# Kernel tuning notes

Measured on AMD Instinct MI355X. Metric: run time of the kernel, lower is better.

Reference implementation:

```python
import jax, jax.numpy as jnp
import numpy as np

B, K, D_MODEL = 64, 256, 512
D_STATE, D_CONV, EXPAND = 16, 4, 1
D_INNER = EXPAND * D_MODEL
DT_RANK = (D_MODEL + 15) // 16  # 32
EPS = 1e-5


def _layer_norm(x, g, b):
    m = jnp.mean(x, axis=-1, keepdims=True)
    v = jnp.mean(jnp.square(x - m), axis=-1, keepdims=True)
    return (x - m) * jax.lax.rsqrt(v + EPS) * g + b


def _silu(x):
    return x * jax.nn.sigmoid(x)


def _mamba_block(x, in_proj_w, conv_w, conv_b, x_proj_w, dt_proj_w, dt_proj_b, A_log, Dp, out_proj_w):
    # x: (B, K, d_model)
    b, k, _ = x.shape
    d_inner = A_log.shape[0]
    d_state = A_log.shape[1]
    dt_rank = dt_proj_w.shape[1]
    xz = x @ in_proj_w.T                      # (B, K, 2*d_inner)
    xi, z = jnp.split(xz, 2, axis=-1)
    # causal depthwise conv1d, width d_conv
    pad = conv_w.shape[1] - 1
    xp = jnp.pad(xi, ((0, 0), (pad, 0), (0, 0)))
    xc = conv_b + sum(xp[:, w:w + k, :] * conv_w[:, w] for w in range(conv_w.shape[1]))
    xc = _silu(xc)
    proj = xc @ x_proj_w.T                    # (B, K, dt_rank + 2*d_state)
    dtr = proj[..., :dt_rank]
    Bc = proj[..., dt_rank:dt_rank + d_state]  # (B, K, d_state)
    Cc = proj[..., dt_rank + d_state:]         # (B, K, d_state)
    dt = jax.nn.softplus(dtr @ dt_proj_w.T + dt_proj_b)  # (B, K, d_inner)
    A = -jnp.exp(A_log)                       # (d_inner, d_state)

    def step(h, inp):
        dt_t, x_t, B_t, C_t = inp             # (B,d_inner),(B,d_inner),(B,d_state),(B,d_state)
        dA = jnp.exp(dt_t[:, :, None] * A)    # (B, d_inner, d_state)
        h = dA * h + (dt_t * x_t)[:, :, None] * B_t[:, None, :]
        y = jnp.einsum('bds,bs->bd', h, C_t)
        return h, y

    h0 = jnp.zeros((b, d_inner, d_state), x.dtype)
    xs = (dt.transpose(1, 0, 2), xc.transpose(1, 0, 2),
          Bc.transpose(1, 0, 2), Cc.transpose(1, 0, 2))
    _, ys = jax.lax.scan(step, h0, xs)        # ys: (K, B, d_inner)
    y = ys.transpose(1, 0, 2) + xc * Dp       # skip term D*x
    y = y * _silu(z)
    return y @ out_proj_w.T


def setup_inputs() -> dict:
    key = jax.random.key(0)
    ks = jax.random.split(key, 8)
    s = 0.02
    slots = jax.random.normal(ks[0], (B, K, D_MODEL), dtype=jnp.float32)
    in_proj_w = jax.random.normal(ks[1], (2 * D_INNER, D_MODEL), jnp.float32) * s
    conv_w = jax.random.normal(ks[2], (D_INNER, D_CONV), jnp.float32) * 0.1
    conv_b = jnp.zeros((D_INNER,), jnp.float32)
    x_proj_w = jax.random.normal(ks[3], (DT_RANK + 2 * D_STATE, D_INNER), jnp.float32) * s
    dt_proj_w = jax.random.normal(ks[4], (D_INNER, DT_RANK), jnp.float32) * s
    dt_proj_b = jax.random.normal(ks[5], (D_INNER,), jnp.float32) * 0.1 - 4.0  # small softplus(dt)
    A_log = jnp.log(jnp.broadcast_to(jnp.arange(1, D_STATE + 1, dtype=jnp.float32), (D_INNER, D_STATE)))
    Dp = jnp.ones((D_INNER,), jnp.float32)
    out_proj_w = jax.random.normal(ks[6], (D_MODEL, D_INNER), jnp.float32) * s
    ln_g = jnp.ones((D_MODEL,), jnp.float32)
    ln_b = jnp.zeros((D_MODEL,), jnp.float32)
    fln_g = jnp.ones((D_MODEL,), jnp.float32)
    fln_b = jnp.zeros((D_MODEL,), jnp.float32)
    return {"slots": slots, "ln_g": ln_g, "ln_b": ln_b,
            "in_proj_w": in_proj_w, "conv_w": conv_w, "conv_b": conv_b,
            "x_proj_w": x_proj_w, "dt_proj_w": dt_proj_w, "dt_proj_b": dt_proj_b,
            "A_log": A_log, "Dp": Dp, "out_proj_w": out_proj_w,
            "fln_g": fln_g, "fln_b": fln_b}


def reference(slots, ln_g, ln_b, in_proj_w, conv_w, conv_b, x_proj_w,
              dt_proj_w, dt_proj_b, A_log, Dp, out_proj_w, fln_g, fln_b):
    x = slots
    # num_layers = 1: pre-norm -> mamba -> residual
    residual = x
    x = _layer_norm(x, ln_g, ln_b)
    x = _mamba_block(x, in_proj_w, conv_w, conv_b, x_proj_w,
                     dt_proj_w, dt_proj_b, A_log, Dp, out_proj_w)
    x = x + residual
    return _layer_norm(x, fln_g, fln_b)
```

## Files before the change

kernel.cpp:

```cpp
#include <hip/hip_runtime.h>
#include <hip/hip_bf16.h>


#define NTOK 16384
#define DM   512

typedef __attribute__((ext_vector_type(8))) short bf16x8;
typedef __attribute__((ext_vector_type(4))) float f32x4;

__device__ __forceinline__ unsigned short f2bf(float f){
  unsigned int u = __float_as_uint(f);
  u = (u + 0x7fffu + ((u >> 16) & 1u)) >> 16;
  return (unsigned short)u;
}
__device__ __forceinline__ float bfu(unsigned short p){ return __uint_as_float(((unsigned int)p) << 16); }
__device__ __forceinline__ unsigned int pk2(float a, float b){
  return (unsigned int)f2bf(a) | ((unsigned int)f2bf(b) << 16);
}
__device__ __forceinline__ float silu(float a){ return a / (1.f + __expf(-a)); }

__device__ __forceinline__ float qsum(float x){
  x += __int_as_float(__builtin_amdgcn_mov_dpp(__float_as_int(x), 0xB1, 0xF, 0xF, true));
  x += __int_as_float(__builtin_amdgcn_mov_dpp(__float_as_int(x), 0x4E, 0xF, 0xF, true));
  return x;
}

__device__ __forceinline__ void async_cp16(const unsigned short* g, unsigned short* l){
  __builtin_amdgcn_global_load_lds(
      (const __attribute__((address_space(1))) unsigned int*)g,
      (__attribute__((address_space(3))) unsigned int*)l, 16, 0, 0);
}

__global__ __launch_bounds__(256) void k_cvtw(const float* __restrict__ W,
                                              unsigned short* __restrict__ Wb){
  int i = (blockIdx.x*256 + threadIdx.x)*8;
  float4 a = *(const float4*)(W+i);
  float4 b = *(const float4*)(W+i+4);
  uint4 st = { pk2(a.x,a.y), pk2(a.z,a.w), pk2(b.x,b.y), pk2(b.z,b.w) };
  *(uint4*)(Wb+i) = st;
}

__global__ __launch_bounds__(64) void k_ln(const float* __restrict__ x,
                                           const float* __restrict__ g,
                                           const float* __restrict__ b,
                                           unsigned short* __restrict__ out){
  int tok  = blockIdx.x;
  int lane = threadIdx.x;
  const float* row = x + (size_t)tok*DM + lane*8;
  float4 r0 = *(const float4*)row;
  float4 r1 = *(const float4*)(row + 4);
  float v[8] = {r0.x,r0.y,r0.z,r0.w, r1.x,r1.y,r1.z,r1.w};
  float s = 0.f;
  #pragma unroll
  for (int i=0;i<8;i++) s += v[i];
  #pragma unroll
  for (int o=32;o;o>>=1) s += __shfl_xor(s, o, 64);
  float m = s * (1.0f/512.0f);
  float vs = 0.f;
  #pragma unroll
  for (int i=0;i<8;i++){ float d = v[i]-m; vs += d*d; }
  #pragma unroll
  for (int o=32;o;o>>=1) vs += __shfl_xor(vs, o, 64);
  float rs = rsqrtf(vs*(1.0f/512.0f) + 1e-5f);
  float4 g0 = *(const float4*)(g + lane*8);
  float4 g1 = *(const float4*)(g + lane*8 + 4);
  float4 b0 = *(const float4*)(b + lane*8);
  float4 b1 = *(const float4*)(b + lane*8 + 4);
  float gv[8] = {g0.x,g0.y,g0.z,g0.w, g1.x,g1.y,g1.z,g1.w};
  float bv[8] = {b0.x,b0.y,b0.z,b0.w, b1.x,b1.y,b1.z,b1.w};
  float o8[8];
  #pragma unroll
  for (int i=0;i<8;i++) o8[i] = (v[i]-m)*rs*gv[i] + bv[i];
  uint4 st = { pk2(o8[0],o8[1]), pk2(o8[2],o8[3]), pk2(o8[4],o8[5]), pk2(o8[6],o8[7]) };
  *(uint4*)(out + (size_t)tok*DM + lane*8) = st;
}

__global__ __launch_bounds__(256) void k_gemm(const unsigned short* __restrict__ A,
                                              const unsigned short* __restrict__ Wb,
                                              float* __restrict__ out_f,
                                              unsigned short* __restrict__ out_b,
                                              int mode){
  __shared__ unsigned short As[2][128*32];
  __shared__ unsigned short Bs[2][128*32];
  int t0  = blockIdx.x * 128;
  int n0  = blockIdx.y * 128;
  int tid = threadIdx.x;
  int lane = tid & 63;
  int wv  = tid >> 6;
  int mw  = wv & 1, nw = wv >> 1;
  int m15 = lane & 15, quad = lane >> 4;

  int srow   = wv*32 + (lane >> 2);
  int schunk = ((lane & 3) ^ ((lane >> 3) & 3)) * 8;
  const unsigned short* gA = A  + (size_t)(t0 + srow)*DM + schunk;
  const unsigned short* gB = Wb + (size_t)(n0 + srow)*DM + schunk;
  unsigned short* asb0 = &As[0][(wv*32)*32];
  unsigned short* bsb0 = &Bs[0][(wv*32)*32];
  unsigned short* asb1 = &As[1][(wv*32)*32];
  unsigned short* bsb1 = &Bs[1][(wv*32)*32];

  async_cp16(gA,         asb0);
  async_cp16(gA + 16*DM, asb0 + 16*32);
  async_cp16(gB,         bsb0);
  async_cp16(gB + 16*DM, bsb0 + 16*32);

  f32x4 acc[4][4];
  #pragma unroll
  for (int rb=0;rb<4;rb++)
    #pragma unroll
    for (int cb=0;cb<4;cb++) acc[rb][cb] = (f32x4){0.f,0.f,0.f,0.f};

  int rdsw = (quad ^ ((m15 >> 1) & 3)) * 8;
  int cur = 0;
  for (int ks = 0; ks < 16; ks++){
    __syncthreads();
    if (ks < 15){
      const unsigned short* nA = gA + (ks+1)*32;
      const unsigned short* nB = gB + (ks+1)*32;
      unsigned short* na = cur ? asb0 : asb1;
      unsigned short* nb = cur ? bsb0 : bsb1;
      async_cp16(nA,         na);
      async_cp16(nA + 16*DM, na + 16*32);
      async_cp16(nB,         nb);
      async_cp16(nB + 16*DM, nb + 16*32);
    }
    bf16x8 af[4], bfr[4];
    #pragma unroll
    for (int rb=0;rb<4;rb++)
      af[rb] = *(const bf16x8*)&As[cur][(mw*64 + rb*16 + m15)*32 + rdsw];
    #pragma unroll
    for (int cb=0;cb<4;cb++)
      bfr[cb] = *(const bf16x8*)&Bs[cur][(nw*64 + cb*16 + m15)*32 + rdsw];
    #pragma unroll
    for (int rb=0;rb<4;rb++)
      #pragma unroll
      for (int cb=0;cb<4;cb++)
        acc[rb][cb] = __builtin_amdgcn_mfma_f32_16x16x32_bf16(af[rb], bfr[cb], acc[rb][cb], 0, 0, 0);
    cur ^= 1;
  }

  #pragma unroll
  for (int rb=0;rb<4;rb++){
    int tok0 = t0 + mw*64 + rb*16 + quad*4;
    int b    = tok0 >> 8;
    int tl0  = tok0 & 255;
    #pragma unroll
    for (int cb=0;cb<4;cb++){
      int nn = n0 + nw*64 + cb*16 + m15;
      f32x4 v = acc[rb][cb];
      if (mode == 0){
        if (nn < DM){
          *(f32x4*)(out_f + ((size_t)(b*DM + nn))*256 + tl0) = v;
        } else {
          uint2 z2 = { pk2(silu(v[0]), silu(v[1])), pk2(silu(v[2]), silu(v[3])) };
          *(uint2*)(out_b + ((size_t)(b*DM + (nn - DM)))*256 + tl0) = z2;
        }
      } else {
        #pragma unroll
        for (int r=0;r<4;r++) out_f[(size_t)(tok0+r)*DM + nn] = v[r];
      }
    }
  }
}

__global__ __launch_bounds__(256) void k_xproj(const float* __restrict__ xiT,
                                               const float* __restrict__ cw,
                                               const float* __restrict__ cb,
                                               const unsigned short* __restrict__ xpwb,
                                               const unsigned short* __restrict__ dtwb,
                                               const float* __restrict__ dtb,
                                               unsigned short* __restrict__ dtTb,
                                               unsigned short* __restrict__ xcT,
                                               float* __restrict__ Bc,
                                               float* __restrict__ Cc){
  __shared__ unsigned short xcb[32*520];
  __shared__ unsigned short pjA[32*40];
  int t0  = blockIdx.x * 32;
  int b   = t0 >> 8;
  int tl0 = t0 & 255;
  int tid = threadIdx.x;
  int lane = tid & 63;
  int wv  = tid >> 6;
  int m15 = lane & 15, quad = lane >> 4;

  #pragma unroll
  for (int j=0;j<2;j++){
    int d = tid + 256*j;
    float4 cr = *(const float4*)(cw + d*4);
    float a0 = cb[d];
    const float* row = xiT + ((size_t)(b*DM + d))*256;
    float w[36];
    if (tl0 == 0){
      w[0]=w[1]=w[2]=w[3]=0.f;
      #pragma unroll
      for (int q2=0;q2<8;q2++){
        float4 v4 = *(const float4*)(row + q2*4);
        w[4+q2*4]=v4.x; w[5+q2*4]=v4.y; w[6+q2*4]=v4.z; w[7+q2*4]=v4.w;
      }
    } else {
      const float* p4 = row + tl0 - 4;
      #pragma unroll
      for (int q2=0;q2<9;q2++){
        float4 v4 = *(const float4*)(p4 + q2*4);
        w[q2*4]=v4.x; w[1+q2*4]=v4.y; w[2+q2*4]=v4.z; w[3+q2*4]=v4.w;
      }
    }
    unsigned int pkv[16];
    #pragma unroll
    for (int t=0;t<32;t+=2){
      float s0 = silu(a0 + w[t+1]*cr.x + w[t+2]*cr.y + w[t+3]*cr.z + w[t+4]*cr.w);
      float s1 = silu(a0 + w[t+2]*cr.x + w[t+3]*cr.y + w[t+4]*cr.z + w[t+5]*cr.w);
      unsigned int pp = pk2(s0, s1);
      xcb[t*520 + d]     = (unsigned short)pp;
      xcb[(t+1)*520 + d] = (unsigned short)(pp >> 16);
      pkv[t>>1] = pp;
    }
    unsigned short* xr = xcT + ((size_t)(b*DM + d))*256 + tl0;
    *(uint4*)(xr)      = (uint4){ pkv[0],  pkv[1],  pkv[2],  pkv[3]  };
    *(uint4*)(xr + 8)  = (uint4){ pkv[4],  pkv[5],  pkv[6],  pkv[7]  };
    *(uint4*)(xr + 16) = (uint4){ pkv[8],  pkv[9],  pkv[10], pkv[11] };
    *(uint4*)(xr + 24) = (uint4){ pkv[12], pkv[13], pkv[14], pkv[15] };
  }
  __syncthreads();

  int mt = wv & 1, ntp = wv >> 1;
  f32x4 pacc0 = (f32x4){0.f,0.f,0.f,0.f};
  f32x4 pacc1 = (f32x4){0.f,0.f,0.f,0.f};
  #pragma unroll 4
  for (int ks=0; ks<16; ks++){
    bf16x8 af = *(const bf16x8*)&xcb[(mt*16 + m15)*520 + ks*32 + quad*8];
    bf16x8 b0 = *(const bf16x8*)(xpwb + (size_t)((ntp*2+0)*16 + m15)*DM + ks*32 + quad*8);
    bf16x8 b1 = *(const bf16x8*)(xpwb + (size_t)((ntp*2+1)*16 + m15)*DM + ks*32 + quad*8);
    pacc0 = __builtin_amdgcn_mfma_f32_16x16x32_bf16(af, b0, pacc0, 0, 0, 0);
    pacc1 = __builtin_amdgcn_mfma_f32_16x16x32_bf16(af, b1, pacc1, 0, 0, 0);
  }

  if (ntp == 0){
    #pragma unroll
    for (int r=0;r<4;r++){
      pjA[(mt*16 + quad*4 + r)*40 + m15]      = f2bf(pacc0[r]);
      pjA[(mt*16 + quad*4 + r)*40 + 16 + m15] = f2bf(pacc1[r]);
    }
  } else {
    #pragma unroll
    for (int r=0;r<4;r++){
      int tt = t0 + mt*16 + quad*4 + r;
      Bc[(size_t)tt*16 + m15] = pacc0[r];
      Cc[(size_t)tt*16 + m15] = pacc1[r];
    }
  }
  __syncthreads();

  bf16x8 adt = *(const bf16x8*)&pjA[(mt*16 + m15)*40 + quad*8];
  int nh = wv >> 1;
  #pragma unroll
  for (int j2=0;j2<16;j2++){
    int nn = (nh*16 + j2)*16 + m15;
    bf16x8 bfr = *(const bf16x8*)(dtwb + nn*32 + quad*8);
    f32x4 dacc = (f32x4){0.f,0.f,0.f,0.f};
    dacc = __builtin_amdgcn_mfma_f32_16x16x32_bf16(adt, bfr, dacc, 0, 0, 0);
    float bb = dtb[nn];
    float s0 = dacc[0] + bb, s1 = dacc[1] + bb, s2 = dacc[2] + bb, s3 = dacc[3] + bb;
    float o0 = (s0 > 20.f) ? s0 : log1pf(__expf(s0));
    float o1 = (s1 > 20.f) ? s1 : log1pf(__expf(s1));
    float o2 = (s2 > 20.f) ? s2 : log1pf(__expf(s2));
    float o3 = (s3 > 20.f) ? s3 : log1pf(__expf(s3));
    *(uint2*)(dtTb + ((size_t)(b*DM + nn))*256 + tl0 + mt*16 + quad*4)
        = (uint2){ pk2(o0,o1), pk2(o2,o3) };
  }
}

#define SCAN_STEP(DV, UV, BV, CV, ZS, OUT) do {                                 \
    float dv_ = (DV);                                                           \
    float u_  = (UV);                                                           \
    float du_ = dv_*u_;                                                         \
    h0 = fmaf(exp2f(dv_*A0), h0, du_*(BV).x);                                   \
    h1 = fmaf(exp2f(dv_*A1), h1, du_*(BV).y);                                   \
    h2 = fmaf(exp2f(dv_*A2), h2, du_*(BV).z);                                   \
    h3 = fmaf(exp2f(dv_*A3), h3, du_*(BV).w);                                   \
    float yy_ = fmaf(h3,(CV).w, fmaf(h2,(CV).z, fmaf(h1,(CV).y, h0*(CV).x)));   \
    yy_ = qsum(yy_);                                                            \
    OUT = fmaf(u_, Dv, yy_) * (ZS);                                             \
  } while(0)

#define SCAN_LOAD(DD, UU, ZZ, B0,B1,B2,B3, C0,C1,C2,C3) do {                    \
    DD  = *(const uint2*)dtp;  UU = *(const uint2*)xup;                         \
    ZZ  = *(const uint2*)zsp;                                                   \
    B0 = *(const float4*)(Bp);    B1 = *(const float4*)(Bp+16);                 \
    B2 = *(const float4*)(Bp+32); B3 = *(const float4*)(Bp+48);                 \
    C0 = *(const float4*)(Cp);    C1 = *(const float4*)(Cp+16);                 \
    C2 = *(const float4*)(Cp+32); C3 = *(const float4*)(Cp+48);                 \
    dtp += 4; xup += 4; zsp += 4; Bp += 64; Cp += 64;                           \
  } while(0)

#define SCAN_BODY(DD, UU, ZZ, B0,B1,B2,B3, C0,C1,C2,C3) do {                    \
    float dv0_ = __uint_as_float((DD).x << 16);                                 \
    float dv1_ = __uint_as_float((DD).x & 0xffff0000u);                         \
    float dv2_ = __uint_as_float((DD).y << 16);                                 \
    float dv3_ = __uint_as_float((DD).y & 0xffff0000u);                         \
    float u0_ = __uint_as_float((UU).x << 16);                                  \
    float u1_ = __uint_as_float((UU).x & 0xffff0000u);                          \
    float u2_ = __uint_as_float((UU).y << 16);                                  \
    float u3_ = __uint_as_float((UU).y & 0xffff0000u);                          \
    float zs0_ = __uint_as_float((ZZ).x << 16);                                 \
    float zs1_ = __uint_as_float((ZZ).x & 0xffff0000u);                         \
    float zs2_ = __uint_as_float((ZZ).y << 16);                                 \
    float zs3_ = __uint_as_float((ZZ).y & 0xffff0000u);                         \
    float o0_,o1_,o2_,o3_;                                                      \
    SCAN_STEP(dv0_,u0_,B0,C0,zs0_,o0_);                                         \
    SCAN_STEP(dv1_,u1_,B1,C1,zs1_,o1_);                                         \
    SCAN_STEP(dv2_,u2_,B2,C2,zs2_,o2_);                                         \
    SCAN_STEP(dv3_,u3_,B3,C3,zs3_,o3_);                                         \
    float osel_ = (sl==0)?o0_:(sl==1)?o1_:(sl==2)?o2_:o3_;                      \
    *yo = f2bf(osel_);                                                          \
    yo += 4*DM;                                                                 \
  } while(0)

__global__ __launch_bounds__(256) void k_scan(const unsigned short* __restrict__ dtT,
                                              const unsigned short* __restrict__ xcT,
                                              const unsigned short* __restrict__ zsT,
                                              const float* __restrict__ Bc,
                                              const float* __restrict__ Cc,
                                              const float* __restrict__ Alog,
                                              const float* __restrict__ Dpw,
                                              unsigned short* __restrict__ ya){
  int tid = threadIdx.x;
  int sl  = tid & 3;
  int q   = blockIdx.x*64 + (tid >> 2);
  int d   = q & 511;
  int b   = q >> 9;
  const float LOG2E = 1.44269504f;
  float4 Alr = *(const float4*)(Alog + d*16 + sl*4);
  float A0 = -__expf(Alr.x)*LOG2E, A1 = -__expf(Alr.y)*LOG2E;
  float A2 = -__expf(Alr.z)*LOG2E, A3 = -__expf(Alr.w)*LOG2E;
  float Dv = Dpw[d];
  float h0=0.f, h1=0.f, h2=0.f, h3=0.f;
  const unsigned short* dtp = dtT + (size_t)q*256;
  const unsigned short* xup = xcT + (size_t)q*256;
  const unsigned short* zsp = zsT + (size_t)q*256;
  unsigned short* yo = ya + (size_t)b*256*DM + d + sl*DM;
  const float* Bp = Bc + (size_t)b*4096 + sl*4;
  const float* Cp = Cc + (size_t)b*4096 + sl*4;

  uint2 ddA, uuA, zzA; float4 a0,a1,a2,a3, e0,e1,e2,e3;
  uint2 ddB, uuB, zzB; float4 f0,f1,f2,f3, g0,g1,g2,g3;

  SCAN_LOAD(ddA,uuA,zzA, a0,a1,a2,a3, e0,e1,e2,e3);
  for (int it = 0; it < 64; it += 2){
    SCAN_LOAD(ddB,uuB,zzB, f0,f1,f2,f3, g0,g1,g2,g3);
    SCAN_BODY(ddA,uuA,zzA, a0,a1,a2,a3, e0,e1,e2,e3);
    if (it < 62)
      SCAN_LOAD(ddA,uuA,zzA, a0,a1,a2,a3, e0,e1,e2,e3);
    SCAN_BODY(ddB,uuB,zzB, f0,f1,f2,f3, g0,g1,g2,g3);
  }
}

__global__ __launch_bounds__(64) void k_fln(const float* __restrict__ o,
                                            const float* __restrict__ resid,
                                            const float* __restrict__ g,
                                            const float* __restrict__ b,
                                            float* __restrict__ out){
  int tok  = blockIdx.x;
  int lane = threadIdx.x;
  const float* row = o     + (size_t)tok*DM + lane*8;
  const float* rr  = resid + (size_t)tok*DM + lane*8;
  float4 r0 = *(const float4*)row;
  float4 r1 = *(const float4*)(row + 4);
  float4 s0 = *(const float4*)rr;
  float4 s1 = *(const float4*)(rr + 4);
  float v[8] = {r0.x+s0.x, r0.y+s0.y, r0.z+s0.z, r0.w+s0.w,
                r1.x+s1.x, r1.y+s1.y, r1.z+s1.z, r1.w+s1.w};
  float s = 0.f;
  #pragma unroll
  for (int i=0;i<8;i++) s += v[i];
  #pragma unroll
  for (int o2=32;o2;o2>>=1) s += __shfl_xor(s, o2, 64);
  float m = s * (1.0f/512.0f);
  float vs = 0.f;
  #pragma unroll
  for (int i=0;i<8;i++){ float d = v[i]-m; vs += d*d; }
  #pragma unroll
  for (int o2=32;o2;o2>>=1) vs += __shfl_xor(vs, o2, 64);
  float rs = rsqrtf(vs*(1.0f/512.0f) + 1e-5f);
  float4 g0 = *(const float4*)(g + lane*8);
  float4 g1 = *(const float4*)(g + lane*8 + 4);
  float4 b0 = *(const float4*)(b + lane*8);
  float4 b1 = *(const float4*)(b + lane*8 + 4);
  float gv[8] = {g0.x,g0.y,g0.z,g0.w, g1.x,g1.y,g1.z,g1.w};
  float bv[8] = {b0.x,b0.y,b0.z,b0.w, b1.x,b1.y,b1.z,b1.w};
  float o8[8];
  #pragma unroll
  for (int i=0;i<8;i++) o8[i] = (v[i]-m)*rs*gv[i] + bv[i];
  float4* op = (float4*)(out + (size_t)tok*DM + lane*8);
  op[0] = make_float4(o8[0],o8[1],o8[2],o8[3]);
  op[1] = make_float4(o8[4],o8[5],o8[6],o8[7]);
}

extern "C" void kernel_launch(void* const* d_in, const int* in_sizes, int n_in,
                              void* d_out, int out_size, void* d_ws, size_t ws_size,
                              hipStream_t stream) {
  const float* slots     = (const float*)d_in[0];
  const float* ln_g      = (const float*)d_in[1];
  const float* ln_b      = (const float*)d_in[2];
  const float* in_proj_w = (const float*)d_in[3];
  const float* conv_w    = (const float*)d_in[4];
  const float* conv_b    = (const float*)d_in[5];
  const float* x_proj_w  = (const float*)d_in[6];
  const float* dt_proj_w = (const float*)d_in[7];
  const float* dt_proj_b = (const float*)d_in[8];
  const float* A_log     = (const float*)d_in[9];
  const float* Dp        = (const float*)d_in[10];
  const float* out_projw = (const float*)d_in[11];
  const float* fln_g     = (const float*)d_in[12];
  const float* fln_b     = (const float*)d_in[13];
  float* out = (float*)d_out;

  const size_t MB = 1024*1024;
  char* base = (char*)d_ws;
  float*          xiT  = (float*)(base);
  unsigned short* xlnb = (unsigned short*)(base + 32*MB);
  unsigned short* yab  = xlnb;
  unsigned short* xpwb = xlnb;
  unsigned short* dtwb = xlnb + 32768;
  unsigned short* zsT  = (unsigned short*)(base + 48*MB);
  unsigned short* WbO  = zsT;
  unsigned short* dtTb = (unsigned short*)(base + 64*MB);
  unsigned short* xcT  = (unsigned short*)(base + 80*MB);
  float*          dto  = (float*)(base + 64*MB);
  unsigned short* WbI  = (unsigned short*)dto;
  float*          Bc   = (float*)(base + 96*MB);
  float*          Cc   = (float*)(base + 97*MB);

  k_ln   <<<NTOK,           64, 0, stream>>>(slots, ln_g, ln_b, xlnb);
  k_cvtw <<<256,           256, 0, stream>>>(in_proj_w, WbI);
  k_gemm <<<dim3(128, 8),  256, 0, stream>>>(xlnb, WbI, xiT, zsT, 0);
  k_cvtw <<<16,            256, 0, stream>>>(x_proj_w, xpwb);
  k_cvtw <<<8,             256, 0, stream>>>(dt_proj_w, dtwb);
  k_xproj<<<NTOK/32,       256, 0, stream>>>(xiT, conv_w, conv_b, xpwb, dtwb, dt_proj_b,
                                             dtTb, xcT, Bc, Cc);
  k_scan <<<512,           256, 0, stream>>>(dtTb, xcT, zsT, Bc, Cc, A_log, Dp, yab);
  k_cvtw <<<128,           256, 0, stream>>>(out_projw, WbO);
  k_gemm <<<dim3(128, 4),  256, 0, stream>>>(yab, WbO, dto, (unsigned short*)0, 1);
  k_fln  <<<NTOK,           64, 0, stream>>>(dto, slots, fln_g, fln_b, out);
}
```

Baseline: 302.6 us.

## Store xi token-major from in_proj GEMM and rework conv to read row-major

The in_proj GEMM now writes the xi half in token-major (token, channel) layout instead of the transposed channel-major layout. The conv+SiLU stage in k_xproj is restructured so each thread handles four adjacent channels over 16 tokens, sliding a 4-tap window down rows and reading coalesced float4 loads. This changes how the GEMM epilogue and the conv prologue interact. The intent is cheaper, coalesced conv loads, at the cost of scalar strided stores in the GEMM epilogue.

```diff
diff --git a/kernel.cpp b/kernel.cpp
--- a/kernel.cpp
+++ b/kernel.cpp
@@ -150,7 +150,8 @@
       f32x4 v = acc[rb][cb];
       if (mode == 0){
         if (nn < DM){
-          *(f32x4*)(out_f + ((size_t)(b*DM + nn))*256 + tl0) = v;
+          #pragma unroll
+          for (int r=0;r<4;r++) out_f[(size_t)(tok0+r)*DM + nn] = v[r];
         } else {
           uint2 z2 = { pk2(silu(v[0]), silu(v[1])), pk2(silu(v[2]), silu(v[3])) };
           *(uint2*)(out_b + ((size_t)(b*DM + (nn - DM)))*256 + tl0) = z2;
@@ -163,7 +164,7 @@
   }
 }
 
-__global__ __launch_bounds__(256) void k_xproj(const float* __restrict__ xiT,
+__global__ __launch_bounds__(256) void k_xproj(const float* __restrict__ xi,
                                                const float* __restrict__ cw,
                                                const float* __restrict__ cb,
                                                const unsigned short* __restrict__ xpwb,
@@ -175,51 +176,64 @@
                                                float* __restrict__ Cc){
   __shared__ unsigned short xcb[32*520];
   __shared__ unsigned short pjA[32*40];
-  int t0  = blockIdx.x * 32;
-  int b   = t0 >> 8;
-  int tl0 = t0 & 255;
+  int t0g = blockIdx.x * 32;
+  int b   = t0g >> 8;
+  int tl0 = t0g & 255;
   int tid = threadIdx.x;
   int lane = tid & 63;
   int wv  = tid >> 6;
   int m15 = lane & 15, quad = lane >> 4;
 
-  #pragma unroll
-  for (int j=0;j<2;j++){
-    int d = tid + 256*j;
-    float4 cr = *(const float4*)(cw + d*4);
-    float a0 = cb[d];
-    const float* row = xiT + ((size_t)(b*DM + d))*256;
-    float w[36];
-    if (tl0 == 0){
-      w[0]=w[1]=w[2]=w[3]=0.f;
-      #pragma unroll
-      for (int q2=0;q2<8;q2++){
-        float4 v4 = *(const float4*)(row + q2*4);
-        w[4+q2*4]=v4.x; w[5+q2*4]=v4.y; w[6+q2*4]=v4.z; w[7+q2*4]=v4.w;
-      }
+  {
+    int dq = tid & 127, tg = tid >> 7;
+    int d4 = dq * 4;
+    int gt0 = t0g + tg*16;
+    const float* xr = xi + (size_t)gt0*DM + d4;
+    float4 cw0 = *(const float4*)(cw + (d4+0)*4);
+    float4 cw1 = *(const float4*)(cw + (d4+1)*4);
+    float4 cw2 = *(const float4*)(cw + (d4+2)*4);
+    float4 cw3 = *(const float4*)(cw + (d4+3)*4);
+    float4 cb4 = *(const float4*)(cb + d4);
+    float4 w3, w2, w1;
+    if (tl0 == 0 && tg == 0){
+      w3 = make_float4(0,0,0,0); w2 = w3; w1 = w3;
     } else {
-      const float* p4 = row + tl0 - 4;
-      #pragma unroll
-      for (int q2=0;q2<9;q2++){
-        float4 v4 = *(const float4*)(p4 + q2*4);
-        w[q2*4]=v4.x; w[1+q2*4]=v4.y; w[2+q2*4]=v4.z; w[3+q2*4]=v4.w;
-      }
-    }
-    unsigned int pkv[16];
-    #pragma unroll
-    for (int t=0;t<32;t+=2){
-      float s0 = silu(a0 + w[t+1]*cr.x + w[t+2]*cr.y + w[t+3]*cr.z + w[t+4]*cr.w);
-      float s1 = silu(a0 + w[t+2]*cr.x + w[t+3]*cr.y + w[t+4]*cr.z + w[t+5]*cr.w);
-      unsigned int pp = pk2(s0, s1);
-      xcb[t*520 + d]     = (unsigned short)pp;
-      xcb[(t+1)*520 + d] = (unsigned short)(pp >> 16);
-      pkv[t>>1] = pp;
-    }
-    unsigned short* xr = xcT + ((size_t)(b*DM + d))*256 + tl0;
-    *(uint4*)(xr)      = (uint4){ pkv[0],  pkv[1],  pkv[2],  pkv[3]  };
-    *(uint4*)(xr + 8)  = (uint4){ pkv[4],  pkv[5],  pkv[6],  pkv[7]  };
-    *(uint4*)(xr + 16) = (uint4){ pkv[8],  pkv[9],  pkv[10], pkv[11] };
-    *(uint4*)(xr + 24) = (uint4){ pkv[12], pkv[13], pkv[14], pkv[15] };
+      w3 = *(const float4*)(xr - 3*DM);
+      w2 = *(const float4*)(xr - 2*DM);
+      w1 = *(const float4*)(xr - 1*DM);
+    }
+    unsigned int q0[8], q1[8], q2[8], q3[8];
+    float p0=0.f, p1=0.f, p2=0.f, p3=0.f;
+    #pragma unroll
+    for (int t=0;t<16;t++){
+      float4 w0 = *(const float4*)(xr + (size_t)t*DM);
+      float a0 = cb4.x + w3.x*cw0.x + w2.x*cw0.y + w1.x*cw0.z + w0.x*cw0.w;
+      float a1 = cb4.y + w3.y*cw1.x + w2.y*cw1.y + w1.y*cw1.z + w0.y*cw1.w;
+      float a2 = cb4.z + w3.z*cw2.x + w2.z*cw2.y + w1.z*cw2.z + w0.z*cw2.w;
+      float a3 = cb4.w + w3.w*cw3.x + w2.w*cw3.y + w1.w*cw3.z + w0.w*cw3.w;
+      float s0 = silu(a0), s1 = silu(a1), s2 = silu(a2), s3 = silu(a3);
+      *(uint2*)&xcb[(tg*16 + t)*520 + d4] = (uint2){ pk2(s0,s1), pk2(s2,s3) };
+      if (t & 1){
+        q0[t>>1] = pk2(p0, s0);
+        q1[t>>1] = pk2(p1, s1);
+        q2[t>>1] = pk2(p2, s2);
+        q3[t>>1] = pk2(p3, s3);
+      } else { p0=s0; p1=s1; p2=s2; p3=s3; }
+      w3 = w2; w2 = w1; w1 = w0;
+    }
+    int tlg = tl0 + tg*16;
+    unsigned short* x0 = xcT + ((size_t)(b*DM + d4+0))*256 + tlg;
+    unsigned short* x1 = xcT + ((size_t)(b*DM + d4+1))*256 + tlg;
+    unsigned short* x2 = xcT + ((size_t)(b*DM + d4+2))*256 + tlg;
+    unsigned short* x3 = xcT + ((size_t)(b*DM + d4+3))*256 + tlg;
+    *(uint4*)(x0)     = (uint4){ q0[0], q0[1], q0[2], q0[3] };
+    *(uint4*)(x0 + 8) = (uint4){ q0[4], q0[5], q0[6], q0[7] };
+    *(uint4*)(x1)     = (uint4){ q1[0], q1[1], q1[2], q1[3] };
+    *(uint4*)(x1 + 8) = (uint4){ q1[4], q1[5], q1[6], q1[7] };
+    *(uint4*)(x2)     = (uint4){ q2[0], q2[1], q2[2], q2[3] };
+    *(uint4*)(x2 + 8) = (uint4){ q2[4], q2[5], q2[6], q2[7] };
+    *(uint4*)(x3)     = (uint4){ q3[0], q3[1], q3[2], q3[3] };
+    *(uint4*)(x3 + 8) = (uint4){ q3[4], q3[5], q3[6], q3[7] };
   }
   __syncthreads();
 
@@ -244,7 +258,7 @@
   } else {
     #pragma unroll
     for (int r=0;r<4;r++){
-      int tt = t0 + mt*16 + quad*4 + r;
+      int tt = t0g + mt*16 + quad*4 + r;
       Bc[(size_t)tt*16 + m15] = pacc0[r];
       Cc[(size_t)tt*16 + m15] = pacc1[r];
     }
@@ -417,7 +431,7 @@
 
   const size_t MB = 1024*1024;
   char* base = (char*)d_ws;
-  float*          xiT  = (float*)(base);
+  float*          xi   = (float*)(base);
   unsigned short* xlnb = (unsigned short*)(base + 32*MB);
   unsigned short* yab  = xlnb;
   unsigned short* xpwb = xlnb;
@@ -433,10 +447,10 @@
 
   k_ln   <<<NTOK,           64, 0, stream>>>(slots, ln_g, ln_b, xlnb);
   k_cvtw <<<256,           256, 0, stream>>>(in_proj_w, WbI);
-  k_gemm <<<dim3(128, 8),  256, 0, stream>>>(xlnb, WbI, xiT, zsT, 0);
+  k_gemm <<<dim3(128, 8),  256, 0, stream>>>(xlnb, WbI, xi, zsT, 0);
   k_cvtw <<<16,            256, 0, stream>>>(x_proj_w, xpwb);
   k_cvtw <<<8,             256, 0, stream>>>(dt_proj_w, dtwb);
-  k_xproj<<<NTOK/32,       256, 0, stream>>>(xiT, conv_w, conv_b, xpwb, dtwb, dt_proj_b,
+  k_xproj<<<NTOK/32,       256, 0, stream>>>(xi, conv_w, conv_b, xpwb, dtwb, dt_proj_b,
                                              dtTb, xcT, Bc, Cc);
   k_scan <<<512,           256, 0, stream>>>(dtTb, xcT, zsT, Bc, Cc, A_log, Dp, yab);
   k_cvtw <<<128,           256, 0, stream>>>(out_projw, WbO);
```

New measurement: 410.8 us. 1.36x slower.
